# Kernel optimization log

Measured on AMD Instinct MI355X. Metric: run time of the kernel, lower is better.

The kernel has to match this reference:

```python
import jax, jax.numpy as jnp
import numpy as np
from jax import lax

ALPHA = 2.0        # elastic_alpha per axis
SMOOTH_NUM = 4
WIN = 5            # box smoothing window
FS = 11            # elastic field size per dim
SIZE_O = (128, 128, 128)


def _rodrigues(rot):
    # rot: (N,3) angle-axis -> (N,3,3) rotation matrix, with Taylor fallback near 0
    eps = 1e-6
    theta2 = jnp.sum(rot * rot, axis=1, keepdims=True)            # (N,1)
    theta = jnp.sqrt(jnp.maximum(theta2, eps))                    # safe sqrt
    w = rot / (theta + eps)
    wx, wy, wz = w[:, 0:1], w[:, 1:2], w[:, 2:3]
    c = jnp.cos(theta)
    s = jnp.sin(theta)
    k = 1.0 - c
    Rn = jnp.concatenate([
        c + wx * wx * k, wx * wy * k - wz * s, wy * s + wx * wz * k,
        wz * s + wx * wy * k, c + wy * wy * k, -wx * s + wy * wz * k,
        -wy * s + wx * wz * k, wx * s + wy * wz * k, c + wz * wz * k,
    ], axis=1).reshape(-1, 3, 3)
    rx, ry, rz = rot[:, 0:1], rot[:, 1:2], rot[:, 2:3]
    one = jnp.ones_like(rx)
    Rt = jnp.concatenate([one, -rz, ry, rz, one, -rx, -ry, rx, one],
                         axis=1).reshape(-1, 3, 3)
    mask = (theta2 > eps)[:, :, None]                             # (N,1,1)
    return jnp.where(mask, Rn, Rt)


def _box_smooth(d):
    # replicate-pad + mean box filter (torch __smooth_3d__)
    p = WIN // 2
    dp = jnp.pad(d, ((0, 0), (0, 0), (p, p), (p, p), (p, p)), mode='edge')
    k = jnp.ones((1, 1, WIN, WIN, WIN), d.dtype) / float(WIN ** 3)
    return lax.conv_general_dilated(dp, k, (1, 1, 1), 'VALID',
                                    dimension_numbers=('NCDHW', 'OIDHW', 'NCDHW'))


def _resize1d(x, axis, out_size):
    # linear interpolation along one axis, align_corners=False (torch interpolate)
    in_size = x.shape[axis]
    src = (jnp.arange(out_size, dtype=x.dtype) + 0.5) * (in_size / out_size) - 0.5
    src = jnp.clip(src, 0.0, in_size - 1.0)
    i0 = jnp.floor(src).astype(jnp.int32)
    i1 = jnp.minimum(i0 + 1, in_size - 1)
    w = (src - i0.astype(x.dtype))
    shape = [1] * x.ndim
    shape[axis] = out_size
    w = w.reshape(shape)
    x0 = jnp.take(x, i0, axis=axis)
    x1 = jnp.take(x, i1, axis=axis)
    return x0 * (1.0 - w) + x1 * w


def _resize3d(d, size):
    d = _resize1d(d, 2, size[0])
    d = _resize1d(d, 3, size[1])
    d = _resize1d(d, 4, size[2])
    return d


def _grid_sample3d(vol, grid):
    # vol: (N,C,D,H,W), grid: (N,D,H,W,3) normalized (x,y,z); trilinear, zeros pad,
    # align_corners=False (torch grid_sample defaults)
    N, C, D, H, W = vol.shape
    x = ((grid[..., 0] + 1.0) * W - 1.0) * 0.5
    y = ((grid[..., 1] + 1.0) * H - 1.0) * 0.5
    z = ((grid[..., 2] + 1.0) * D - 1.0) * 0.5
    x0f, y0f, z0f = jnp.floor(x), jnp.floor(y), jnp.floor(z)
    wx, wy, wz = x - x0f, y - y0f, z - z0f
    x0 = x0f.astype(jnp.int32)
    y0 = y0f.astype(jnp.int32)
    z0 = z0f.astype(jnp.int32)
    b = jnp.arange(N)[:, None, None, None]

    def gather(zi, yi, xi):
        valid = (zi >= 0) & (zi < D) & (yi >= 0) & (yi < H) & (xi >= 0) & (xi < W)
        v = vol[b, :, jnp.clip(zi, 0, D - 1), jnp.clip(yi, 0, H - 1),
                jnp.clip(xi, 0, W - 1)]                           # (N,Do,Ho,Wo,C)
        return v * valid[..., None].astype(vol.dtype)

    out = (gather(z0, y0, x0) * ((1 - wz) * (1 - wy) * (1 - wx))[..., None]
           + gather(z0, y0, x0 + 1) * ((1 - wz) * (1 - wy) * wx)[..., None]
           + gather(z0, y0 + 1, x0) * ((1 - wz) * wy * (1 - wx))[..., None]
           + gather(z0, y0 + 1, x0 + 1) * ((1 - wz) * wy * wx)[..., None]
           + gather(z0 + 1, y0, x0) * (wz * (1 - wy) * (1 - wx))[..., None]
           + gather(z0 + 1, y0, x0 + 1) * (wz * (1 - wy) * wx)[..., None]
           + gather(z0 + 1, y0 + 1, x0) * (wz * wy * (1 - wx))[..., None]
           + gather(z0 + 1, y0 + 1, x0 + 1) * (wz * wy * wx)[..., None])
    return jnp.transpose(out, (0, 4, 1, 2, 3))


def _field(raw, size):
    # raw uniform field -> scaled, smoothed, cropped, resized displacement (D,H,W)
    d = (raw - 0.5) * 2.0 * ALPHA
    for _ in range(SMOOTH_NUM):
        d = _box_smooth(d)
    p = WIN // 2
    d = d[:, :, p:p + FS, p:p + FS, p:p + FS]
    return _resize3d(d, size)[0, 0]


def _forward(vol, rot, scale, shift, dz, dy, dx):
    N, C, D, H, W = vol.shape
    R = _rodrigues(rot)                                  # (N,3,3)
    A = R * scale[:, None, :]                            # scale multiplies columns
    theta = jnp.concatenate([A, shift[:, :, None]], axis=2)  # (N,3,4)
    # base affine grid, align_corners=False: coord_i = (2i+1)/S - 1
    xs = (2.0 * jnp.arange(W, dtype=vol.dtype) + 1.0) / W - 1.0
    ys = (2.0 * jnp.arange(H, dtype=vol.dtype) + 1.0) / H - 1.0
    zs = (2.0 * jnp.arange(D, dtype=vol.dtype) + 1.0) / D - 1.0
    zz, yy, xx = jnp.meshgrid(zs, ys, xs, indexing='ij')
    pts = jnp.stack([xx, yy, zz, jnp.ones_like(xx)], axis=-1)    # (D,H,W,4)
    grid = jnp.einsum('nij,dhwj->ndhwi', theta, pts)             # (N,D,H,W,3)
    disp = jnp.stack([_field(dz, (D, H, W)), _field(dy, (D, H, W)),
                      _field(dx, (D, H, W))], axis=-1)           # (D,H,W,3)
    grid = grid + disp[None]
    out = _grid_sample3d(vol, grid)
    # central crop to SIZE_O
    zs0 = D // 2 - SIZE_O[0] // 2
    ys0 = H // 2 - SIZE_O[1] // 2
    xs0 = W // 2 - SIZE_O[2] // 2
    return out[:, :, zs0:zs0 + SIZE_O[0], ys0:ys0 + SIZE_O[1], xs0:xs0 + SIZE_O[2]]


def setup_inputs() -> dict:
    key = jax.random.key(0)
    k = jax.random.split(key, 7)
    vol = jax.random.normal(k[0], (4, 1, 160, 160, 160), dtype=jnp.float32)
    rot = (jax.random.uniform(k[1], (4, 3), dtype=jnp.float32) - 0.5) * 0.35   # ~±10 deg in rad
    scale = 0.9 + 0.2 * jax.random.uniform(k[2], (4, 3), dtype=jnp.float32)
    shift = (jax.random.uniform(k[3], (4, 3), dtype=jnp.float32) - 0.5) * 0.1
    dz = jax.random.uniform(k[4], (1, 1, 15, 15, 15), dtype=jnp.float32)
    dy = jax.random.uniform(k[5], (1, 1, 15, 15, 15), dtype=jnp.float32)
    dx = jax.random.uniform(k[6], (1, 1, 15, 15, 15), dtype=jnp.float32)
    return {"vol": vol, "rot": rot, "scale": scale, "shift": shift,
            "dz": dz, "dy": dy, "dx": dx}


def reference(vol, rot, scale, shift, dz, dy, dx):
    return _forward(vol, rot, scale, shift, dz, dy, dx)
```

## Files before the change

### kernel.cpp

```cpp
#include <hip/hip_runtime.h>

#define VD 160
#define OD 128
#define CROP0 16
#define FSZ 11
#define RAWSZ 15
#define NBATCH 4
#define ODQ 4

#define EPAD 16
#define E_K  (OD*EPAD)
#define E_C  (OD*OD*EPAD)

struct M15 { float v[15][15]; };
constexpr M15 mkB() {
    M15 b{};
    for (int i = 0; i < 15; ++i)
        for (int j = 0; j < 15; ++j) b.v[i][j] = 0.0f;
    for (int i = 0; i < 15; ++i)
        for (int t = -2; t <= 2; ++t) {
            int j = i + t; j = j < 0 ? 0 : (j > 14 ? 14 : j);
            b.v[i][j] += 0.2f;
        }
    return b;
}
constexpr M15 mmul(const M15& a, const M15& b) {
    M15 c{};
    for (int i = 0; i < 15; ++i)
        for (int j = 0; j < 15; ++j) {
            float s = 0.0f;
            for (int k = 0; k < 15; ++k) s += a.v[i][k] * b.v[k][j];
            c.v[i][j] = s;
        }
    return c;
}
constexpr M15 B2 = mmul(mkB(), mkB());
constexpr M15 B4 = mmul(B2, B2);

__global__ __launch_bounds__(1024) void prep_kernel(
        const float* __restrict__ rot, const float* __restrict__ scale,
        const float* __restrict__ shift,
        const float* __restrict__ dz, const float* __restrict__ dy,
        const float* __restrict__ dx,
        float* __restrict__ theta, float* __restrict__ fields) {
    const int tid = threadIdx.x;
    const int chan = blockIdx.x;

    if (chan == 3) {
        int n = tid;
        if (n >= NBATCH) return;
        float rx = rot[n*3+0], ry = rot[n*3+1], rz = rot[n*3+2];
        float t2 = rx*rx + ry*ry + rz*rz;
        const float eps = 1e-6f;
        float th = sqrtf(fmaxf(t2, eps));
        float inv = 1.0f / (th + eps);
        float wx = rx*inv, wy = ry*inv, wz = rz*inv;
        float c = cosf(th), s = sinf(th), k = 1.0f - c;
        float R[9];
        if (t2 > eps) {
            R[0] = c + wx*wx*k;      R[1] = wx*wy*k - wz*s;  R[2] = wy*s + wx*wz*k;
            R[3] = wz*s + wx*wy*k;   R[4] = c + wy*wy*k;     R[5] = -wx*s + wy*wz*k;
            R[6] = -wy*s + wx*wz*k;  R[7] = wx*s + wy*wz*k;  R[8] = c + wz*wz*k;
        } else {
            R[0] = 1.0f; R[1] = -rz;  R[2] = ry;
            R[3] = rz;   R[4] = 1.0f; R[5] = -rx;
            R[6] = -ry;  R[7] = rx;   R[8] = 1.0f;
        }
        for (int i = 0; i < 3; ++i) {
            for (int j = 0; j < 3; ++j)
                theta[n*12 + i*4 + j] = R[i*3 + j] * scale[n*3 + j];
            theta[n*12 + i*4 + 3] = shift[n*3 + i];
        }
        return;
    }

    __shared__ float bufA[RAWSZ*RAWSZ*RAWSZ];
    __shared__ float bufB[RAWSZ*RAWSZ*FSZ];
    __shared__ float bufC[RAWSZ*FSZ*FSZ];
    const float* raw = (chan == 0) ? dz : (chan == 1) ? dy : dx;
    const int NTOT = RAWSZ*RAWSZ*RAWSZ;

    for (int i = tid; i < NTOT; i += 1024)
        bufA[i] = (raw[i] - 0.5f) * 4.0f;
    __syncthreads();

    for (int i = tid; i < RAWSZ*RAWSZ*FSZ; i += 1024) {
        const int zy = i / FSZ;
        const int xo = i % FSZ;
        const float* row = &bufA[zy * RAWSZ];
        const float* w = B4.v[xo + 2];
        float s = 0.0f;
        #pragma unroll
        for (int j = 0; j < RAWSZ; ++j) s += row[j] * w[j];
        bufB[i] = s;
    }
    __syncthreads();

    for (int i = tid; i < RAWSZ*FSZ*FSZ; i += 1024) {
        const int z  = i / (FSZ*FSZ);
        const int r  = i % (FSZ*FSZ);
        const int yo = r / FSZ;
        const int xo = r % FSZ;
        const float* base = &bufB[z * (RAWSZ*FSZ) + xo];
        const float* w = B4.v[yo + 2];
        float s = 0.0f;
        #pragma unroll
        for (int j = 0; j < RAWSZ; ++j) s += base[j * FSZ] * w[j];
        bufC[i] = s;
    }
    __syncthreads();

    for (int i = tid; i < FSZ*FSZ*FSZ; i += 1024) {
        const int zo = i / (FSZ*FSZ);
        const int r  = i % (FSZ*FSZ);
        const float* base = &bufC[r];
        const float* w = B4.v[zo + 2];
        float s = 0.0f;
        #pragma unroll
        for (int j = 0; j < RAWSZ; ++j) s += base[j * (FSZ*FSZ)] * w[j];
        fields[chan*FSZ*FSZ*FSZ + i] = s;
    }
}

__device__ __forceinline__ void resize_coord(int m, int& i0, int& i1, float& w) {
    float s = fmaf((float)m + 0.5f, (float)FSZ / (float)VD, -0.5f);
    s = fminf(fmaxf(s, 0.0f), (float)(FSZ - 1));
    float f = floorf(s);
    i0 = (int)f;
    i1 = min(i0 + 1, FSZ - 1);
    w = s - f;
}

__global__ __launch_bounds__(128) void etab_kernel(
        const float* __restrict__ fields, float* __restrict__ etab) {
    const int od = blockIdx.x;
    const int oh = threadIdx.x;
    int zi0, zi1, yi0, yi1; float zw, yw;
    resize_coord(od + CROP0, zi0, zi1, zw);
    resize_coord(oh + CROP0, yi0, yi1, yw);
    const float w00 = (1.0f-zw)*(1.0f-yw), w01 = (1.0f-zw)*yw;
    const float w10 = zw*(1.0f-yw),        w11 = zw*yw;
    #pragma unroll
    for (int c = 0; c < 3; ++c) {
        const float* f = fields + c * (FSZ*FSZ*FSZ);
        const float* r00 = f + zi0*121 + yi0*11;
        const float* r01 = f + zi0*121 + yi1*11;
        const float* r10 = f + zi1*121 + yi0*11;
        const float* r11 = f + zi1*121 + yi1*11;
        float vv[EPAD];
        #pragma unroll
        for (int xi = 0; xi < FSZ; ++xi)
            vv[xi] = 80.0f * (r00[xi]*w00 + r01[xi]*w01 + r10[xi]*w10 + r11[xi]*w11);
        #pragma unroll
        for (int xi = FSZ; xi < EPAD; ++xi) vv[xi] = 0.0f;
        float4* dst = (float4*)(etab + ((size_t)c*OD + od)*E_K + (size_t)oh*EPAD);
        #pragma unroll
        for (int q = 0; q < EPAD/4; ++q)
            dst[q] = make_float4(vv[4*q], vv[4*q+1], vv[4*q+2], vv[4*q+3]);
    }
}

__global__ __launch_bounds__(512, 4) void sample_kernel(
        const float* __restrict__ vol, const float* __restrict__ theta,
        const float* __restrict__ etab, float* __restrict__ out) {
    const int tid  = threadIdx.x;
    const int lane = tid & 63;
    const int wl   = lane & 15;
    const int hl   = lane >> 4;
    const int wv   = tid >> 6;
    const int wx   = wv & 1;
    const int wh   = (wv >> 1) & 1;
    const int wd   = wv >> 2;

    const int ow   = (blockIdx.x << 5) | (wx << 4) | wl;
    const int oh   = (blockIdx.y << 3) | (wh << 2) | hl;
    const int odb  = (blockIdx.z & 15) << 3;
    const int n    = blockIdx.z >> 4;
    const int od0  = odb + (wd << 2);

    const int w_ = ow + CROP0;

    const float x = fmaf(2.0f * (float)w_ + 1.0f, 1.0f / (float)VD, -1.0f);
    const float y = fmaf(2.0f * (float)(oh + CROP0) + 1.0f, 1.0f / (float)VD, -1.0f);

    float s = fmaf((float)w_ + 0.5f, (float)FSZ / (float)VD, -0.5f);
    s = fminf(fmaxf(s, 0.0f), (float)(FSZ - 1));
    const float sf = floorf(s);
    const int   xi0 = (int)sf;
    const float xw  = s - sf;

    const float* th = theta + n*12;
    const float cx = fmaf(th[0]*x + th[1]*y + th[3], 80.0f, 79.5f);
    const float cy = fmaf(th[4]*x + th[5]*y + th[7], 80.0f, 79.5f);
    const float cz = fmaf(th[8]*x + th[9]*y + th[11], 80.0f, 79.5f);
    const float tz0 = th[2] * 80.0f, tz1 = th[6] * 80.0f, tz2 = th[10] * 80.0f;

    const float* v = vol + (size_t)n * (VD*VD*VD);

    const float* ep = etab + (size_t)od0*E_K + (size_t)oh*EPAD + xi0;
    float e0[3][ODQ], e1[3][ODQ];
    #pragma unroll
    for (int c = 0; c < 3; ++c)
        #pragma unroll
        for (int k = 0; k < ODQ; ++k) {
            e0[c][k] = ep[c*E_C + k*E_K    ];
            e1[c][k] = ep[c*E_C + k*E_K + 1];
        }
    __builtin_amdgcn_sched_barrier(0);

    const float zb = fmaf(2.0f * (float)(od0 + CROP0) + 1.0f,
                          1.0f / (float)VD, -1.0f);
    float fx[ODQ], fy[ODQ], fz[ODQ];
    int ix[ODQ], iy[ODQ], iz[ODQ];
    int inb = 1;
    #pragma unroll
    for (int k = 0; k < ODQ; ++k) {
        const float z = zb + (float)k * (2.0f / (float)VD);
        const float d80x = fmaf(e1[0][k] - e0[0][k], xw, e0[0][k]);
        const float d80y = fmaf(e1[1][k] - e0[1][k], xw, e0[1][k]);
        const float d80z = fmaf(e1[2][k] - e0[2][k], xw, e0[2][k]);
        const float xs = fmaf(tz0, z, cx) + d80x;
        const float ys = fmaf(tz1, z, cy) + d80y;
        const float zs = fmaf(tz2, z, cz) + d80z;
        const float x0f = floorf(xs), y0f = floorf(ys), z0f = floorf(zs);
        fx[k] = xs - x0f; fy[k] = ys - y0f; fz[k] = zs - z0f;
        ix[k] = (int)x0f; iy[k] = (int)y0f; iz[k] = (int)z0f;
        inb &= ((unsigned)ix[k] < (unsigned)(VD-1)) &
               ((unsigned)iy[k] < (unsigned)(VD-1)) &
               ((unsigned)iz[k] < (unsigned)(VD-1));
    }

    float* op = out + ((((size_t)n*OD + od0)*OD + oh)*OD + ow);

    if (__all(inb)) {
        float2 p00[ODQ], p01[ODQ], p10[ODQ], p11[ODQ];
        #pragma unroll
        for (int k = 0; k < ODQ; ++k) {
            const int b00 = (iz[k]*VD + iy[k])*VD + ix[k];
            __builtin_memcpy(&p00[k], v + b00,            sizeof(float2));
            __builtin_memcpy(&p01[k], v + b00 + VD,       sizeof(float2));
            __builtin_memcpy(&p10[k], v + b00 + VD*VD,    sizeof(float2));
            __builtin_memcpy(&p11[k], v + b00 + VD*VD+VD, sizeof(float2));
        }
        __builtin_amdgcn_sched_barrier(0);
        #pragma unroll
        for (int k = 0; k < ODQ; ++k) {
            const float r00 = fmaf(fx[k], p00[k].y - p00[k].x, p00[k].x);
            const float r01 = fmaf(fx[k], p01[k].y - p01[k].x, p01[k].x);
            const float r10 = fmaf(fx[k], p10[k].y - p10[k].x, p10[k].x);
            const float r11 = fmaf(fx[k], p11[k].y - p11[k].x, p11[k].x);
            const float r0 = fmaf(fy[k], r01 - r00, r00);
            const float r1 = fmaf(fy[k], r11 - r10, r10);
            op[(size_t)k*OD*OD] = fmaf(fz[k], r1 - r0, r0);
        }
    } else {
        #pragma unroll
        for (int k = 0; k < ODQ; ++k) {
            const int ix1 = ix[k] + 1, iy1 = iy[k] + 1, iz1 = iz[k] + 1;

            const float WX0 = ((unsigned)ix[k] < (unsigned)VD) ? (1.0f - fx[k]) : 0.0f;
            const float WX1 = ((unsigned)ix1   < (unsigned)VD) ? fx[k]          : 0.0f;
            const float WY0 = ((unsigned)iy[k] < (unsigned)VD) ? (1.0f - fy[k]) : 0.0f;
            const float WY1 = ((unsigned)iy1   < (unsigned)VD) ? fy[k]          : 0.0f;
            const float WZ0 = ((unsigned)iz[k] < (unsigned)VD) ? (1.0f - fz[k]) : 0.0f;
            const float WZ1 = ((unsigned)iz1   < (unsigned)VD) ? fz[k]          : 0.0f;

            const int xc0 = min(max(ix[k], 0), VD-1), xc1 = min(max(ix1, 0), VD-1);
            const int yc0 = min(max(iy[k], 0), VD-1), yc1 = min(max(iy1, 0), VD-1);
            const int zc0 = min(max(iz[k], 0), VD-1), zc1 = min(max(iz1, 0), VD-1);

            const int base = min(xc0, VD-2);
            const bool hi0 = (xc0 != base);
            const bool hi1 = (xc1 != base);
            const float wA = (hi0 ? 0.0f : WX0) + (hi1 ? 0.0f : WX1);
            const float wB = (hi0 ? WX0 : 0.0f) + (hi1 ? WX1 : 0.0f);

            const int sA = zc0*(VD*VD), sB = zc1*(VD*VD);
            const int tA = yc0*VD + base, tB = yc1*VD + base;

            float2 p00, p01, p10, p11;
            __builtin_memcpy(&p00, v + sA + tA, sizeof(float2));
            __builtin_memcpy(&p01, v + sA + tB, sizeof(float2));
            __builtin_memcpy(&p10, v + sB + tA, sizeof(float2));
            __builtin_memcpy(&p11, v + sB + tB, sizeof(float2));

            const float r00 = p00.x*wA + p00.y*wB;
            const float r01 = p01.x*wA + p01.y*wB;
            const float r10 = p10.x*wA + p10.y*wB;
            const float r11 = p11.x*wA + p11.y*wB;
            op[(size_t)k*OD*OD] = (r00*WY0 + r01*WY1)*WZ0 + (r10*WY0 + r11*WY1)*WZ1;
        }
    }
}

extern "C" void kernel_launch(void* const* d_in, const int* in_sizes, int n_in,
                              void* d_out, int out_size, void* d_ws, size_t ws_size,
                              hipStream_t stream) {
    const float* vol   = (const float*)d_in[0];
    const float* rot   = (const float*)d_in[1];
    const float* scale = (const float*)d_in[2];
    const float* shift = (const float*)d_in[3];
    const float* dz    = (const float*)d_in[4];
    const float* dy    = (const float*)d_in[5];
    const float* dx    = (const float*)d_in[6];
    float* out = (float*)d_out;

    float* ws     = (float*)d_ws;
    float* theta  = ws;
    float* fields = ws + 48;
    float* etab   = ws + 4096;

    prep_kernel<<<4, 1024, 0, stream>>>(rot, scale, shift, dz, dy, dx,
                                        theta, fields);
    etab_kernel<<<OD, 128, 0, stream>>>(fields, etab);
    dim3 grid(OD/32, OD/8, (OD/8)*NBATCH);
    sample_kernel<<<grid, 512, 0, stream>>>(vol, theta, etab, out);
}
```

Measured before the change: 148.7 us.

## Fuse elastic table build into sample kernel via shared memory and retile blocks

Removes the separate etab_kernel launch and its global table. Each sample block now interpolates its own slice of the displacement field from the 11^3 fields into shared memory and reads it back after a barrier. The block tile changes from 32x8 to 64 wide by 4 high in W/H, so each wavefront covers one contiguous 64-element output row. An empty asm also forces the gathered voxel loads to complete before the interpolation math. This saves one launch and the global round trip for the table, at the cost of redundant per-block field interpolation and a __syncthreads.

```diff
diff --git a/kernel.cpp b/kernel.cpp
--- a/kernel.cpp
+++ b/kernel.cpp
@@ -8,9 +8,8 @@
 #define NBATCH 4
 #define ODQ 4
 
-#define EPAD 16
-#define E_K  (OD*EPAD)
-#define E_C  (OD*OD*EPAD)
+#define ESTR 17
+#define E_CST (32*ESTR)
 
 struct M15 { float v[15][15]; };
 constexpr M15 mkB() {
@@ -131,52 +130,44 @@
     w = s - f;
 }
 
-__global__ __launch_bounds__(128) void etab_kernel(
-        const float* __restrict__ fields, float* __restrict__ etab) {
-    const int od = blockIdx.x;
-    const int oh = threadIdx.x;
-    int zi0, zi1, yi0, yi1; float zw, yw;
-    resize_coord(od + CROP0, zi0, zi1, zw);
-    resize_coord(oh + CROP0, yi0, yi1, yw);
-    const float w00 = (1.0f-zw)*(1.0f-yw), w01 = (1.0f-zw)*yw;
-    const float w10 = zw*(1.0f-yw),        w11 = zw*yw;
-    #pragma unroll
-    for (int c = 0; c < 3; ++c) {
-        const float* f = fields + c * (FSZ*FSZ*FSZ);
-        const float* r00 = f + zi0*121 + yi0*11;
-        const float* r01 = f + zi0*121 + yi1*11;
-        const float* r10 = f + zi1*121 + yi0*11;
-        const float* r11 = f + zi1*121 + yi1*11;
-        float vv[EPAD];
-        #pragma unroll
-        for (int xi = 0; xi < FSZ; ++xi)
-            vv[xi] = 80.0f * (r00[xi]*w00 + r01[xi]*w01 + r10[xi]*w10 + r11[xi]*w11);
-        #pragma unroll
-        for (int xi = FSZ; xi < EPAD; ++xi) vv[xi] = 0.0f;
-        float4* dst = (float4*)(etab + ((size_t)c*OD + od)*E_K + (size_t)oh*EPAD);
-        #pragma unroll
-        for (int q = 0; q < EPAD/4; ++q)
-            dst[q] = make_float4(vv[4*q], vv[4*q+1], vv[4*q+2], vv[4*q+3]);
-    }
-}
-
 __global__ __launch_bounds__(512, 4) void sample_kernel(
         const float* __restrict__ vol, const float* __restrict__ theta,
-        const float* __restrict__ etab, float* __restrict__ out) {
+        const float* __restrict__ fields, float* __restrict__ out) {
+    __shared__ float e[3*E_CST];
+
     const int tid  = threadIdx.x;
     const int lane = tid & 63;
-    const int wl   = lane & 15;
-    const int hl   = lane >> 4;
     const int wv   = tid >> 6;
-    const int wx   = wv & 1;
-    const int wh   = (wv >> 1) & 1;
+    const int oh_l = wv & 3;
     const int wd   = wv >> 2;
 
-    const int ow   = (blockIdx.x << 5) | (wx << 4) | wl;
-    const int oh   = (blockIdx.y << 3) | (wh << 2) | hl;
+    const int ow   = (blockIdx.x << 6) | lane;
+    const int oh   = (blockIdx.y << 2) | oh_l;
     const int odb  = (blockIdx.z & 15) << 3;
     const int n    = blockIdx.z >> 4;
     const int od0  = odb + (wd << 2);
+
+    {
+        const int xi = tid & 15;
+        const int rb = tid >> 4;
+        if (xi < FSZ) {
+            const int od_l  = rb & 7;
+            const int oh_l2 = rb >> 3;
+            int zi0, zi1, yi0, yi1; float zw, yw;
+            resize_coord(odb + od_l + CROP0, zi0, zi1, zw);
+            resize_coord((blockIdx.y << 2) + oh_l2 + CROP0, yi0, yi1, yw);
+            const float w00 = (1.0f-zw)*(1.0f-yw), w01 = (1.0f-zw)*yw;
+            const float w10 = zw*(1.0f-yw),        w11 = zw*yw;
+            const int o00 = zi0*121 + yi0*11 + xi, o01 = zi0*121 + yi1*11 + xi;
+            const int o10 = zi1*121 + yi0*11 + xi, o11 = zi1*121 + yi1*11 + xi;
+            #pragma unroll
+            for (int c = 0; c < 3; ++c) {
+                const float* f = fields + c * (FSZ*FSZ*FSZ);
+                e[(c*32 + rb)*ESTR + xi] =
+                    80.0f * (f[o00]*w00 + f[o01]*w01 + f[o10]*w10 + f[o11]*w11);
+            }
+        }
+    }
 
     const int w_ = ow + CROP0;
 
@@ -197,19 +188,23 @@
 
     const float* v = vol + (size_t)n * (VD*VD*VD);
 
-    const float* ep = etab + (size_t)od0*E_K + (size_t)oh*EPAD + xi0;
+    const float* ebase = &e[(oh_l*8 + (wd << 2))*ESTR + xi0];
+
+    const float zb = fmaf(2.0f * (float)(od0 + CROP0) + 1.0f,
+                          1.0f / (float)VD, -1.0f);
+    float* op = out + ((((size_t)n*OD + od0)*OD + oh)*OD + ow);
+
+    __syncthreads();
+
     float e0[3][ODQ], e1[3][ODQ];
     #pragma unroll
     for (int c = 0; c < 3; ++c)
         #pragma unroll
         for (int k = 0; k < ODQ; ++k) {
-            e0[c][k] = ep[c*E_C + k*E_K    ];
-            e1[c][k] = ep[c*E_C + k*E_K + 1];
-        }
-    __builtin_amdgcn_sched_barrier(0);
-
-    const float zb = fmaf(2.0f * (float)(od0 + CROP0) + 1.0f,
-                          1.0f / (float)VD, -1.0f);
+            e0[c][k] = ebase[c*E_CST + k*ESTR    ];
+            e1[c][k] = ebase[c*E_CST + k*ESTR + 1];
+        }
+
     float fx[ODQ], fy[ODQ], fz[ODQ];
     int ix[ODQ], iy[ODQ], iz[ODQ];
     int inb = 1;
@@ -230,8 +225,6 @@
                ((unsigned)iz[k] < (unsigned)(VD-1));
     }
 
-    float* op = out + ((((size_t)n*OD + od0)*OD + oh)*OD + ow);
-
     if (__all(inb)) {
         float2 p00[ODQ], p01[ODQ], p10[ODQ], p11[ODQ];
         #pragma unroll
@@ -243,6 +236,12 @@
             __builtin_memcpy(&p11[k], v + b00 + VD*VD+VD, sizeof(float2));
         }
         __builtin_amdgcn_sched_barrier(0);
+        #pragma unroll
+        for (int k = 0; k < ODQ; ++k)
+            asm volatile("" :: "v"(p00[k].x), "v"(p00[k].y),
+                               "v"(p01[k].x), "v"(p01[k].y),
+                               "v"(p10[k].x), "v"(p10[k].y),
+                               "v"(p11[k].x), "v"(p11[k].y));
         #pragma unroll
         for (int k = 0; k < ODQ; ++k) {
             const float r00 = fmaf(fx[k], p00[k].y - p00[k].x, p00[k].x);
@@ -308,11 +307,9 @@
     float* ws     = (float*)d_ws;
     float* theta  = ws;
     float* fields = ws + 48;
-    float* etab   = ws + 4096;
 
     prep_kernel<<<4, 1024, 0, stream>>>(rot, scale, shift, dz, dy, dx,
                                         theta, fields);
-    etab_kernel<<<OD, 128, 0, stream>>>(fields, etab);
-    dim3 grid(OD/32, OD/8, (OD/8)*NBATCH);
-    sample_kernel<<<grid, 512, 0, stream>>>(vol, theta, etab, out);
-}
+    dim3 grid(OD/64, OD/4, (OD/8)*NBATCH);
+    sample_kernel<<<grid, 512, 0, stream>>>(vol, theta, fields, out);
+}
```

After: 139.2 us, median of 2. 6.4% less time.
